# Optimization experiments

Measured on AMD Instinct MI355X. Metric: run time of the kernel, lower is better.

## Reference

```python
import jax, jax.numpy as jnp
import numpy as np

B, S, E, H, D, L, V, O = 64, 512, 512, 8, 64, 4, 50000, 1000
KW, STRIDE = 5, 5
L_OUT = (S - KW) // STRIDE + 1  # 102


def setup_inputs() -> dict:
    key = jax.random.key(0)
    ks = jax.random.split(key, 20)
    sc = 0.02
    inp = {
        'tokens': jax.random.randint(ks[0], (B, S), 0, V, dtype=jnp.int32),
        'emb': jax.random.normal(ks[1], (V + 1, E), jnp.float32) * sc,
        'Wq': jax.random.normal(ks[2], (L, H, E, D), jnp.float32) * sc,
        'bq': jnp.zeros((L, H, D), jnp.float32),
        'Wk': jax.random.normal(ks[3], (L, H, E, D), jnp.float32) * sc,
        'bk': jnp.zeros((L, H, D), jnp.float32),
        'Wv': jax.random.normal(ks[4], (L, H, E, D), jnp.float32) * sc,
        'bv': jnp.zeros((L, H, D), jnp.float32),
        'Wo': jax.random.normal(ks[5], (L, H * D, E), jnp.float32) * sc,
        'bo': jnp.zeros((L, E), jnp.float32),
        'W1': jax.random.normal(ks[6], (L, E, 2 * E), jnp.float32) * sc,
        'b1': jnp.zeros((L, 2 * E), jnp.float32),
        'W2': jax.random.normal(ks[7], (L, 2 * E, E), jnp.float32) * sc,
        'b2': jnp.zeros((L, E), jnp.float32),
        'Wc': jax.random.normal(ks[8], (KW, E, 1), jnp.float32) * sc,
        'bc': jnp.zeros((1,), jnp.float32),
        'Wd': jax.random.normal(ks[9], (L_OUT, O), jnp.float32) * sc,
        'bd': jnp.zeros((O,), jnp.float32),
    }
    return inp


def _l2_normalize(x, eps=1e-12):
    # tf.math.l2_normalize: x / sqrt(max(sum(x^2), eps))
    sq = jnp.sum(x * x, axis=-1, keepdims=True)
    return x * jax.lax.rsqrt(jnp.maximum(sq, eps))


def _forward(tokens, emb, Wq, bq, Wk, bk, Wv, bv, Wo, bo, W1, b1, W2, b2, Wc, bc, Wd, bd):
    mask = jnp.sign(tokens).astype(jnp.float32)[..., None]  # [B,S,1]
    out = emb[tokens] * mask                                 # [B,S,E]
    scale = 1.0 / jnp.sqrt(jnp.float32(E))                   # note: scaled by EMBEDDING_DIM, as in source
    for i in range(L):
        # per-head QKV projections, batched over heads
        q = jnp.einsum('bse,hed->bhsd', out, Wq[i]) + bq[i][None, :, None, :]
        k = jnp.einsum('bse,hed->bhsd', out, Wk[i]) + bk[i][None, :, None, :]
        v = jnp.einsum('bse,hed->bhsd', out, Wv[i]) + bv[i][None, :, None, :]
        scores = jnp.einsum('bhsd,bhtd->bhst', q, k) * scale
        attn = jax.nn.softmax(scores, axis=-1)
        heads = jnp.einsum('bhst,bhtd->bhsd', attn, v)       # [B,H,S,D]
        cat = heads.transpose(0, 2, 1, 3).reshape(B, S, H * D)
        mh = cat @ Wo[i] + bo[i]
        out = _l2_normalize(out + mh)
        ff = jax.nn.relu(out @ W1[i] + b1[i]) @ W2[i] + b2[i]
        out = ff + out
    # Conv1D(1, 5, strides=5) then squeeze channel, Dense over seq-length axis, softmax
    conv = jax.lax.conv_general_dilated(
        out, Wc, window_strides=(STRIDE,), padding='VALID',
        dimension_numbers=('NWC', 'WIO', 'NWC')) + bc          # [B,L_OUT,1]
    pooled = jnp.squeeze(conv, axis=-1)                        # [B,L_OUT]
    logits = pooled @ Wd + bd                                  # [B,O]
    return jax.nn.softmax(logits, axis=-1)


def reference(tokens, emb, Wq, bq, Wk, bk, Wv, bv, Wo, bo, W1, b1, W2, b2, Wc, bc, Wd, bd):
    return _forward(tokens, emb, Wq, bq, Wk, bk, Wv, bv, Wo, bo, W1, b1, W2, b2, Wc, bc, Wd, bd)
```

## Files before the change

kernel.cpp:

```cpp
#include <hip/hip_runtime.h>
#include <cstddef>

constexpr int B_ = 64, S_ = 512, E_ = 512, H_ = 8, D_ = 64, L_ = 4, O_ = 1000;
constexpr int BS_ = B_ * S_;
constexpr int HD_ = H_ * D_;
constexpr int QS_ = 1536;
constexpr int LOUT_ = 102;
constexpr float SCALE_ = 0.04419417382415922f;

typedef __bf16 bf16x8 __attribute__((ext_vector_type(8)));
typedef __bf16 bf16x4 __attribute__((ext_vector_type(4)));
typedef __bf16 bf16x2 __attribute__((ext_vector_type(2)));
typedef float floatx4 __attribute__((ext_vector_type(4)));

__device__ inline void load16_lds(const __bf16* g, __bf16* l) {
  __builtin_amdgcn_global_load_lds(
      (const __attribute__((address_space(1))) void*)g,
      (__attribute__((address_space(3))) void*)l, 16, 0, 0);
}

__global__ __launch_bounds__(256) void transpose_bf16(
    const float* __restrict__ in, __bf16* __restrict__ out,
    int R, int C, int IZ, int OZL, int OZH) {
  __shared__ float t[32][33];
  int z = blockIdx.z;
  const float* inz = in + (size_t)z * IZ;
  __bf16* outz = out + (size_t)(z >> 3) * OZL + (size_t)(z & 7) * OZH;
  int c0 = blockIdx.x * 32, r0 = blockIdx.y * 32;
  int x = threadIdx.x, y = threadIdx.y;
#pragma unroll
  for (int j = 0; j < 32; j += 8) t[y + j][x] = inz[(size_t)(r0 + y + j) * C + c0 + x];
  __syncthreads();
#pragma unroll
  for (int j = 0; j < 32; j += 8)
    outz[(size_t)(c0 + y + j) * R + r0 + x] = (__bf16)t[x][y + j];
}

__global__ __launch_bounds__(256) void bias_concat(
    const float* __restrict__ bq, const float* __restrict__ bk,
    const float* __restrict__ bv, float* __restrict__ qkvb) {
  int idx = blockIdx.x * 256 + threadIdx.x;
  int l = idx / QS_, j = idx % QS_;
  float v;
  if (j < 512) v = bq[l * 512 + j];
  else if (j < 1024) v = bk[l * 512 + j - 512];
  else v = bv[l * 512 + j - 1024];
  qkvb[idx] = v;
}

__global__ __launch_bounds__(256) void embed_kernel(
    const int* __restrict__ tokens, const float* __restrict__ emb,
    float* __restrict__ X, __bf16* __restrict__ Ab) {
  int idx = blockIdx.x * 256 + threadIdx.x;
  int bs = idx >> 7;
  int e = (idx & 127) << 2;
  int tok = tokens[bs];
  float4 v;
  if (tok == 0) v = make_float4(0.f, 0.f, 0.f, 0.f);
  else v = *(const float4*)(emb + (size_t)tok * E_ + e);
  size_t off = (size_t)bs * E_ + e;
  *(float4*)(X + off) = v;
  bf16x4 b;
  b[0] = (__bf16)v.x; b[1] = (__bf16)v.y; b[2] = (__bf16)v.z; b[3] = (__bf16)v.w;
  *(bf16x4*)(Ab + off) = b;
}

template <int RELU, int RES, int OUTF, int OUTB, int SCQ, int KITER>
__global__ __launch_bounds__(256) void gemm_bf16(
    const __bf16* __restrict__ A, const __bf16* __restrict__ Bt,
    const float* __restrict__ bias, const float* __restrict__ Rsd,
    float* __restrict__ Cf, __bf16* __restrict__ Cb, int N, int lda, int Nt) {
  __shared__ __align__(16) __bf16 smem[128 * 136];
  __bf16* As = smem;
  __bf16* Bs = smem + 8192;
  int tid = threadIdx.x;
  int lane = tid & 63, w = tid >> 6;
  int Mt8 = (int)(gridDim.x / Nt) >> 3;
  int xcd = blockIdx.x & 7;
  int j = blockIdx.x >> 3;
  int rr = j % (2 * Nt), chunk = j / (2 * Nt);
  int mt = xcd * Mt8 + chunk * 2 + (rr & 1);
  int nt = rr >> 1;
  int m0 = mt * 128, n0 = nt * 128;
  int q4 = lane >> 4, a_ = lane & 15;
  floatx4 acc[4][4];
#pragma unroll
  for (int i = 0; i < 4; ++i)
#pragma unroll
    for (int jj = 0; jj < 4; ++jj) acc[i][jj] = (floatx4)(0.0f);

  for (int kk = 0; kk < KITER; ++kk) {
    int k0 = kk * 64;
#pragma unroll
    for (int jj = 0; jj < 4; ++jj) {
      int ci = (jj * 4 + w) * 64 + lane;
      int row = ci >> 3, c = ci & 7, q = c ^ (row & 7);
      load16_lds(A + (size_t)(m0 + row) * lda + k0 + q * 8, As + (size_t)(jj * 4 + w) * 512);
    }
#pragma unroll
    for (int jj = 0; jj < 4; ++jj) {
      int ci = (jj * 4 + w) * 64 + lane;
      int row = ci >> 3, c = ci & 7, q = c ^ (row & 7);
      load16_lds(Bt + (size_t)(n0 + row) * (KITER * 64) + k0 + q * 8,
                 Bs + (size_t)(jj * 4 + w) * 512);
    }
    __syncthreads();
#pragma unroll
    for (int ks = 0; ks < 2; ++ks) {
      bf16x8 af[4], bfr[4];
#pragma unroll
      for (int i = 0; i < 4; ++i) {
        int row = (w & 1) * 64 + i * 16 + a_;
        int q = ks * 4 + q4;
        af[i] = *(const bf16x8*)&As[(row * 8 + (q ^ (row & 7))) * 8];
      }
#pragma unroll
      for (int jc = 0; jc < 4; ++jc) {
        int row = (w >> 1) * 64 + jc * 16 + a_;
        int q = ks * 4 + q4;
        bfr[jc] = *(const bf16x8*)&Bs[(row * 8 + (q ^ (row & 7))) * 8];
      }
#pragma unroll
      for (int i = 0; i < 4; ++i)
#pragma unroll
        for (int jc = 0; jc < 4; ++jc)
          acc[i][jc] = __builtin_amdgcn_mfma_f32_16x16x32_bf16(bfr[jc], af[i],
                                                               acc[i][jc], 0, 0, 0);
    }
    __syncthreads();
  }
#pragma unroll
  for (int i = 0; i < 4; ++i) {
    int ml = (w & 1) * 64 + i * 16 + a_;
    int m = m0 + ml;
#pragma unroll
    for (int jc = 0; jc < 4; ++jc) {
      int nl = (w >> 1) * 64 + jc * 16 + q4 * 4;
      int n = n0 + nl;
      float4 bi = *(const float4*)(bias + n);
      floatx4 v = acc[i][jc];
      v[0] += bi.x; v[1] += bi.y; v[2] += bi.z; v[3] += bi.w;
      if (SCQ) { if (n < 512) v *= SCALE_; }
      if (RES) {
        float4 rv = *(const float4*)(Rsd + (size_t)m * N + n);
        v[0] += rv.x; v[1] += rv.y; v[2] += rv.z; v[3] += rv.w;
      }
      if (RELU) {
#pragma unroll
        for (int r = 0; r < 4; ++r) v[r] = fmaxf(v[r], 0.f);
      }
      if (OUTF) {
        float4 o = make_float4(v[0], v[1], v[2], v[3]);
        *(float4*)(Cf + (size_t)m * N + n) = o;
      }
      if (OUTB) {
        bf16x4 ob;
#pragma unroll
        for (int r = 0; r < 4; ++r) ob[r] = (__bf16)v[r];
        *(bf16x4*)&smem[ml * 136 + nl] = ob;
      }
    }
  }
  if (OUTB) {
    __syncthreads();
#pragma unroll
    for (int it = 0; it < 8; ++it) {
      int cid = it * 256 + tid;
      int row = cid >> 4, c8 = cid & 15;
      bf16x8 val = *(const bf16x8*)&smem[row * 136 + c8 * 8];
      *(bf16x8*)(Cb + (size_t)(m0 + row) * N + n0 + c8 * 8) = val;
    }
  }
}

__global__ __launch_bounds__(256, 2) void attn_bf16(__bf16* __restrict__ QKV) {
  __shared__ __align__(16) __bf16 Qs[256 * 64];
  __shared__ __align__(16) __bf16 Ks[64 * 64];
  __shared__ __align__(16) __bf16 Vt[64 * 64];
  __shared__ __align__(16) __bf16 Ps[64 * 64];
  int tid = threadIdx.x, lane = tid & 63, w = tid >> 6;
  int q4 = lane >> 4, a_ = lane & 15;
  int s0 = blockIdx.x * 256, h = blockIdx.y, b = blockIdx.z;
  size_t rowbase = (size_t)b * S_ * QS_ + h * 64;
  __bf16* Qg = QKV + rowbase;
  const __bf16* Kg = QKV + rowbase + 512;
  const __bf16* Vg = QKV + rowbase + 1024;
#pragma unroll
  for (int j = 0; j < 8; ++j) {
    int ci = j * 256 + w * 64 + lane;
    int row = ci >> 3, c = ci & 7, q = c ^ (row & 7);
    load16_lds(Qg + (size_t)(s0 + row) * QS_ + q * 8, Qs + (j * 256 + w * 64) * 8);
  }
  float mrow[4], lrow[4];
  floatx4 accO[4][4];
#pragma unroll
  for (int cc = 0; cc < 4; ++cc) {
    mrow[cc] = -3.0e38f; lrow[cc] = 0.f;
#pragma unroll
    for (int jc = 0; jc < 4; ++jc) accO[cc][jc] = (floatx4)(0.0f);
  }

  for (int t0 = 0; t0 < S_; t0 += 64) {
#pragma unroll
    for (int j = 0; j < 2; ++j) {
      int ci = j * 256 + w * 64 + lane;
      int row = ci >> 3, c = ci & 7, q = c ^ (row & 7);
      load16_lds(Kg + (size_t)(t0 + row) * QS_ + q * 8, Ks + (j * 256 + w * 64) * 8);
    }
    {
      int tp = tid & 31, dg = tid >> 5;
      bf16x8 v0 = *(const bf16x8*)(Vg + (size_t)(t0 + 2 * tp) * QS_ + dg * 8);
      bf16x8 v1 = *(const bf16x8*)(Vg + (size_t)(t0 + 2 * tp + 1) * QS_ + dg * 8);
#pragma unroll
      for (int x = 0; x < 8; ++x) {
        int d = dg * 8 + x;
        bf16x2 p; p[0] = v0[x]; p[1] = v1[x];
        *(bf16x2*)&Vt[(d * 8 + ((tp >> 2) ^ (d & 7))) * 8 + (tp & 3) * 2] = p;
      }
    }
    __syncthreads();
    bf16x8 af[2][4], bv[2][4];
#pragma unroll
    for (int ks = 0; ks < 2; ++ks)
#pragma unroll
      for (int jc = 0; jc < 4; ++jc) {
        int row = jc * 16 + a_, q = ks * 4 + q4;
        af[ks][jc] = *(const bf16x8*)&Ks[(row * 8 + (q ^ (row & 7))) * 8];
        bv[ks][jc] = *(const bf16x8*)&Vt[(row * 8 + (q ^ (row & 7))) * 8];
      }
#pragma unroll
    for (int cc = 0; cc < 4; ++cc) {
      int sbase = (cc * 4 + w) * 16;
      floatx4 sc[4];
#pragma unroll
      for (int jc = 0; jc < 4; ++jc) sc[jc] = (floatx4)(0.0f);
#pragma unroll
      for (int ks = 0; ks < 2; ++ks) {
        int row = sbase + a_, q = ks * 4 + q4;
        bf16x8 bq = *(const bf16x8*)&Qs[(row * 8 + (q ^ (row & 7))) * 8];
#pragma unroll
        for (int jc = 0; jc < 4; ++jc)
          sc[jc] = __builtin_amdgcn_mfma_f32_16x16x32_bf16(af[ks][jc], bq,
                                                           sc[jc], 0, 0, 0);
      }
      float mx = sc[0][0];
#pragma unroll
      for (int jc = 0; jc < 4; ++jc)
#pragma unroll
        for (int r = 0; r < 4; ++r) mx = fmaxf(mx, sc[jc][r]);
      mx = fmaxf(mx, __shfl_xor(mx, 16));
      mx = fmaxf(mx, __shfl_xor(mx, 32));
      float mnew = fmaxf(mrow[cc], mx);
      float alpha = __expf(mrow[cc] - mnew);
      mrow[cc] = mnew;
      float ps = 0.f;
      int prow = w * 16 + a_;
#pragma unroll
      for (int jc = 0; jc < 4; ++jc) {
        bf16x4 pb;
#pragma unroll
        for (int r = 0; r < 4; ++r) {
          float p = __expf(sc[jc][r] - mnew);
          ps += p;
          pb[r] = (__bf16)p;
        }
        int pc = jc * 2 + (q4 >> 1);
        *(bf16x4*)&Ps[(prow * 8 + (pc ^ (prow & 7))) * 8 + (q4 & 1) * 4] = pb;
      }
      ps += __shfl_xor(ps, 16);
      ps += __shfl_xor(ps, 32);
      lrow[cc] = lrow[cc] * alpha + ps;
      float aal[4];
#pragma unroll
      for (int r = 0; r < 4; ++r) aal[r] = __shfl(alpha, q4 * 4 + r);
#pragma unroll
      for (int jc = 0; jc < 4; ++jc) {
        floatx4 t = accO[cc][jc];
#pragma unroll
        for (int r = 0; r < 4; ++r) t[r] *= aal[r];
        accO[cc][jc] = t;
      }
#pragma unroll
      for (int ks = 0; ks < 2; ++ks) {
        int q = ks * 4 + q4;
        bf16x8 ap = *(const bf16x8*)&Ps[(prow * 8 + (q ^ (prow & 7))) * 8];
#pragma unroll
        for (int jc = 0; jc < 4; ++jc)
          accO[cc][jc] = __builtin_amdgcn_mfma_f32_16x16x32_bf16(
              ap, bv[ks][jc], accO[cc][jc], 0, 0, 0);
      }
    }
    __syncthreads();
  }
#pragma unroll
  for (int cc = 0; cc < 4; ++cc) {
    float inv = 1.f / lrow[cc];
    float linv[4];
#pragma unroll
    for (int r = 0; r < 4; ++r) linv[r] = __shfl(inv, q4 * 4 + r);
    int srow = s0 + (cc * 4 + w) * 16 + q4 * 4;
#pragma unroll
    for (int r = 0; r < 4; ++r)
#pragma unroll
      for (int jc = 0; jc < 4; ++jc)
        Qg[(size_t)(srow + r) * QS_ + jc * 16 + a_] =
            (__bf16)(accO[cc][jc][r] * linv[r]);
  }
}

__global__ __launch_bounds__(256) void addnorm_kernel(
    float* __restrict__ X, const __bf16* __restrict__ MH, __bf16* __restrict__ Ab) {
  int row = blockIdx.x * 4 + (threadIdx.x >> 6);
  int ln = threadIdx.x & 63;
  size_t off = (size_t)row * E_ + ln * 8;
  float xv[8];
  *(float4*)&xv[0] = *(const float4*)(X + off);
  *(float4*)&xv[4] = *(const float4*)(X + off + 4);
  bf16x8 mh = *(const bf16x8*)(MH + off);
  float ss = 0.f;
#pragma unroll
  for (int j = 0; j < 8; ++j) {
    xv[j] += (float)mh[j];
    ss += xv[j] * xv[j];
  }
#pragma unroll
  for (int o = 1; o < 64; o <<= 1) ss += __shfl_xor(ss, o);
  float inv = rsqrtf(fmaxf(ss, 1e-12f));
  bf16x8 ob;
#pragma unroll
  for (int j = 0; j < 8; ++j) {
    xv[j] *= inv;
    ob[j] = (__bf16)xv[j];
  }
  *(float4*)(X + off) = *(float4*)&xv[0];
  *(float4*)(X + off + 4) = *(float4*)&xv[4];
  *(bf16x8*)(Ab + off) = ob;
}

__global__ __launch_bounds__(256) void conv_pool_kernel(
    const float* __restrict__ X, const float* __restrict__ Wc,
    const float* __restrict__ bc, float* __restrict__ pooled) {
  int wid = blockIdx.x * 4 + (threadIdx.x >> 6);
  int ln = threadIdx.x & 63;
  int b = wid / LOUT_, l = wid % LOUT_;
  const float* xr = X + (size_t)b * S_ * E_ + (size_t)l * 5 * E_;
  float v = 0.f;
#pragma unroll
  for (int j = 0; j < 10; ++j) {
    int i = (j * 64 + ln) * 4;
    float4 x4 = *(const float4*)(xr + i);
    float4 w4 = *(const float4*)(Wc + i);
    v += x4.x * w4.x + x4.y * w4.y + x4.z * w4.z + x4.w * w4.w;
  }
#pragma unroll
  for (int o = 32; o >= 1; o >>= 1) v += __shfl_down(v, o);
  if (ln == 0) pooled[b * LOUT_ + l] = v + bc[0];
}

__global__ __launch_bounds__(256) void dense_softmax_kernel(
    const float* __restrict__ pooled, const float* __restrict__ Wd,
    const float* __restrict__ bd, float* __restrict__ out) {
  __shared__ float pl[LOUT_];
  __shared__ float red[256];
  __shared__ float lg[O_];
  int b = blockIdx.x, tid = threadIdx.x;
  if (tid < LOUT_) pl[tid] = pooled[b * LOUT_ + tid];
  __syncthreads();
  for (int o = tid; o < O_; o += 256) {
    float acc = bd[o];
#pragma unroll 6
    for (int l = 0; l < LOUT_; ++l) acc += pl[l] * Wd[l * O_ + o];
    lg[o] = acc;
  }
  __syncthreads();
  float mx = -3.0e38f;
  for (int o = tid; o < O_; o += 256) mx = fmaxf(mx, lg[o]);
  red[tid] = mx;
  __syncthreads();
  for (int s2 = 128; s2 > 0; s2 >>= 1) {
    if (tid < s2) red[tid] = fmaxf(red[tid], red[tid + s2]);
    __syncthreads();
  }
  mx = red[0];
  __syncthreads();
  float se = 0.f;
  for (int o = tid; o < O_; o += 256) {
    float e = __expf(lg[o] - mx);
    lg[o] = e;
    se += e;
  }
  red[tid] = se;
  __syncthreads();
  for (int s2 = 128; s2 > 0; s2 >>= 1) {
    if (tid < s2) red[tid] += red[tid + s2];
    __syncthreads();
  }
  float inv = 1.f / red[0];
  for (int o = tid; o < O_; o += 256) out[(size_t)b * O_ + o] = lg[o] * inv;
}

extern "C" void kernel_launch(void* const* d_in, const int* in_sizes, int n_in,
                              void* d_out, int out_size, void* d_ws, size_t ws_size,
                              hipStream_t stream) {
  const int* tokens = (const int*)d_in[0];
  const float* emb = (const float*)d_in[1];
  const float* Wq = (const float*)d_in[2];
  const float* bq = (const float*)d_in[3];
  const float* Wk = (const float*)d_in[4];
  const float* bk = (const float*)d_in[5];
  const float* Wv = (const float*)d_in[6];
  const float* bv = (const float*)d_in[7];
  const float* Wo = (const float*)d_in[8];
  const float* bo = (const float*)d_in[9];
  const float* W1 = (const float*)d_in[10];
  const float* b1 = (const float*)d_in[11];
  const float* W2 = (const float*)d_in[12];
  const float* b2 = (const float*)d_in[13];
  const float* Wc = (const float*)d_in[14];
  const float* bc = (const float*)d_in[15];
  const float* Wd = (const float*)d_in[16];
  const float* bd = (const float*)d_in[17];
  float* out = (float*)d_out;

  char* ws = (char*)d_ws;
  float* X = (float*)ws;
  __bf16* Ab = (__bf16*)(ws + 67108864);
  __bf16* QKVb = (__bf16*)(ws + 100663296);
  __bf16* FF1b = QKVb;
  __bf16* MHb = (__bf16*)(ws + 201326592);
  __bf16* Wt = (__bf16*)(ws + 234881024);
  __bf16* Wt_qkv = Wt;
  __bf16* Wt_o = Wt + 3145728;
  __bf16* Wt_1 = Wt + 4194304;
  __bf16* Wt_2 = Wt + 6291456;
  float* qkvbias = (float*)(ws + 251658240);
  float* pooled = qkvbias + 6144;

  dim3 tb(32, 8);
  transpose_bf16<<<dim3(2, 16, 32), tb, 0, stream>>>(Wq, Wt_qkv + 0,      512, 64, 32768, 786432, 32768);
  transpose_bf16<<<dim3(2, 16, 32), tb, 0, stream>>>(Wk, Wt_qkv + 262144, 512, 64, 32768, 786432, 32768);
  transpose_bf16<<<dim3(2, 16, 32), tb, 0, stream>>>(Wv, Wt_qkv + 524288, 512, 64, 32768, 786432, 32768);
  transpose_bf16<<<dim3(16, 16, 4), tb, 0, stream>>>(Wo, Wt_o, 512, 512, 262144, 0, 262144);
  transpose_bf16<<<dim3(32, 16, 4), tb, 0, stream>>>(W1, Wt_1, 512, 1024, 524288, 0, 524288);
  transpose_bf16<<<dim3(16, 32, 4), tb, 0, stream>>>(W2, Wt_2, 1024, 512, 524288, 0, 524288);
  bias_concat<<<dim3(24), dim3(256), 0, stream>>>(bq, bk, bv, qkvbias);

  embed_kernel<<<dim3(BS_ * E_ / 4 / 256), dim3(256), 0, stream>>>(tokens, emb, X, Ab);

  dim3 blk(256);
  for (int i = 0; i < L_; ++i) {
    gemm_bf16<0, 0, 0, 1, 1, 8><<<dim3(256 * 12), blk, 0, stream>>>(
        Ab, Wt_qkv + (size_t)i * 786432, qkvbias + i * QS_, nullptr, nullptr,
        QKVb, QS_, 512, 12);
    attn_bf16<<<dim3(2, 8, 64), blk, 0, stream>>>(QKVb);
    gemm_bf16<0, 0, 0, 1, 0, 8><<<dim3(256 * 4), blk, 0, stream>>>(
        QKVb, Wt_o + (size_t)i * 262144, bo + i * E_, nullptr, nullptr, MHb,
        512, QS_, 4);
    addnorm_kernel<<<dim3(BS_ / 4), blk, 0, stream>>>(X, MHb, Ab);
    gemm_bf16<1, 0, 0, 1, 0, 8><<<dim3(256 * 8), blk, 0, stream>>>(
        Ab, Wt_1 + (size_t)i * 524288, b1 + (size_t)i * 2 * E_, nullptr, nullptr,
        FF1b, 1024, 512, 8);
    gemm_bf16<0, 1, 1, 1, 0, 16><<<dim3(256 * 4), blk, 0, stream>>>(
        FF1b, Wt_2 + (size_t)i * 524288, b2 + (size_t)i * E_, X, X, Ab,
        512, 1024, 4);
  }
  conv_pool_kernel<<<dim3(BS_ * LOUT_ / S_ / 4), blk, 0, stream>>>(X, Wc, bc, pooled);
  dense_softmax_kernel<<<dim3(B_), blk, 0, stream>>>(pooled, Wd, bd, out);
}
```

Baseline: 1.509 ms.

## Triple-buffer GEMM LDS tiles with async prefetch and K-step of 32

Restructures the bf16 GEMM main loop into a three-stage LDS ring buffer with BK=32 tiles. Loads for tile k+2 are issued via global_load_lds before computing tile k, and explicit vmcnt waits replace the two full syncthreads per iteration. The intent is to overlap global-to-LDS traffic with MFMA work instead of stalling on each load. In exchange there are twice as many K iterations with fewer MFMAs each, and a new XOR swizzle on a 4-chunk row layout.

```diff
diff --git a/kernel.cpp b/kernel.cpp
--- a/kernel.cpp
+++ b/kernel.cpp
@@ -65,14 +65,12 @@
   *(bf16x4*)(Ab + off) = b;
 }
 
-template <int RELU, int RES, int OUTF, int OUTB, int SCQ, int KITER>
+template <int RELU, int RES, int OUTF, int OUTB, int SCQ, int KT>
 __global__ __launch_bounds__(256) void gemm_bf16(
     const __bf16* __restrict__ A, const __bf16* __restrict__ Bt,
     const float* __restrict__ bias, const float* __restrict__ Rsd,
     float* __restrict__ Cf, __bf16* __restrict__ Cb, int N, int lda, int Nt) {
-  __shared__ __align__(16) __bf16 smem[128 * 136];
-  __bf16* As = smem;
-  __bf16* Bs = smem + 8192;
+  __shared__ __align__(16) __bf16 smem[24576];
   int tid = threadIdx.x;
   int lane = tid & 63, w = tid >> 6;
   int Mt8 = (int)(gridDim.x / Nt) >> 3;
@@ -83,51 +81,65 @@
   int nt = rr >> 1;
   int m0 = mt * 128, n0 = nt * 128;
   int q4 = lane >> 4, a_ = lane & 15;
+  const int ldb = KT * 32;
+  int r0s = tid >> 2, q0s = (tid & 3) ^ ((r0s >> 1) & 3);
+  int r1s = 64 + (tid >> 2), q1s = (tid & 3) ^ ((r1s >> 1) & 3);
+  const __bf16* Ag = A + (size_t)m0 * lda;
+  const __bf16* Bg = Bt + (size_t)n0 * ldb;
+
   floatx4 acc[4][4];
 #pragma unroll
   for (int i = 0; i < 4; ++i)
 #pragma unroll
     for (int jj = 0; jj < 4; ++jj) acc[i][jj] = (floatx4)(0.0f);
 
-  for (int kk = 0; kk < KITER; ++kk) {
-    int k0 = kk * 64;
-#pragma unroll
-    for (int jj = 0; jj < 4; ++jj) {
-      int ci = (jj * 4 + w) * 64 + lane;
-      int row = ci >> 3, c = ci & 7, q = c ^ (row & 7);
-      load16_lds(A + (size_t)(m0 + row) * lda + k0 + q * 8, As + (size_t)(jj * 4 + w) * 512);
-    }
-#pragma unroll
-    for (int jj = 0; jj < 4; ++jj) {
-      int ci = (jj * 4 + w) * 64 + lane;
-      int row = ci >> 3, c = ci & 7, q = c ^ (row & 7);
-      load16_lds(Bt + (size_t)(n0 + row) * (KITER * 64) + k0 + q * 8,
-                 Bs + (size_t)(jj * 4 + w) * 512);
-    }
-    __syncthreads();
-#pragma unroll
-    for (int ks = 0; ks < 2; ++ks) {
-      bf16x8 af[4], bfr[4];
-#pragma unroll
-      for (int i = 0; i < 4; ++i) {
-        int row = (w & 1) * 64 + i * 16 + a_;
-        int q = ks * 4 + q4;
-        af[i] = *(const bf16x8*)&As[(row * 8 + (q ^ (row & 7))) * 8];
-      }
-#pragma unroll
-      for (int jc = 0; jc < 4; ++jc) {
-        int row = (w >> 1) * 64 + jc * 16 + a_;
-        int q = ks * 4 + q4;
-        bfr[jc] = *(const bf16x8*)&Bs[(row * 8 + (q ^ (row & 7))) * 8];
-      }
-#pragma unroll
-      for (int i = 0; i < 4; ++i)
-#pragma unroll
-        for (int jc = 0; jc < 4; ++jc)
-          acc[i][jc] = __builtin_amdgcn_mfma_f32_16x16x32_bf16(bfr[jc], af[i],
-                                                               acc[i][jc], 0, 0, 0);
-    }
-    __syncthreads();
+  auto STAGE = [&](int kt, int bs) {
+    __bf16* Ad = smem + bs * 4096;
+    __bf16* Bd = smem + 12288 + bs * 4096;
+    int k0 = kt * 32;
+    load16_lds(Ag + (size_t)r0s * lda + k0 + q0s * 8, Ad + tid * 8);
+    load16_lds(Ag + (size_t)r1s * lda + k0 + q1s * 8, Ad + (256 + tid) * 8);
+    load16_lds(Bg + (size_t)r0s * ldb + k0 + q0s * 8, Bd + tid * 8);
+    load16_lds(Bg + (size_t)r1s * ldb + k0 + q1s * 8, Bd + (256 + tid) * 8);
+  };
+
+  STAGE(0, 0);
+  if (KT > 1) STAGE(1, 1);
+#pragma unroll
+  for (int kt = 0; kt < KT; ++kt) {
+    if (kt + 2 < KT) {
+      STAGE(kt + 2, (kt + 2) % 3);
+      asm volatile("s_waitcnt vmcnt(8)" ::: "memory");
+    } else if (kt + 1 < KT) {
+      asm volatile("s_waitcnt vmcnt(4)" ::: "memory");
+    } else {
+      asm volatile("s_waitcnt vmcnt(0)" ::: "memory");
+    }
+    __builtin_amdgcn_s_barrier();
+    __builtin_amdgcn_sched_barrier(0);
+    const __bf16* As = smem + (kt % 3) * 4096;
+    const __bf16* Bs = smem + 12288 + (kt % 3) * 4096;
+    bf16x8 af[4], bfr[4];
+#pragma unroll
+    for (int i = 0; i < 4; ++i) {
+      int row = (w & 1) * 64 + i * 16 + a_;
+      int pc = q4 ^ ((row >> 1) & 3);
+      af[i] = *(const bf16x8*)&As[(row * 4 + pc) * 8];
+    }
+#pragma unroll
+    for (int jc = 0; jc < 4; ++jc) {
+      int row = (w >> 1) * 64 + jc * 16 + a_;
+      int pc = q4 ^ ((row >> 1) & 3);
+      bfr[jc] = *(const bf16x8*)&Bs[(row * 4 + pc) * 8];
+    }
+#pragma unroll
+    for (int i = 0; i < 4; ++i)
+#pragma unroll
+      for (int jc = 0; jc < 4; ++jc)
+        acc[i][jc] = __builtin_amdgcn_mfma_f32_16x16x32_bf16(bfr[jc], af[i],
+                                                             acc[i][jc], 0, 0, 0);
+    asm volatile("" ::: "memory");
+    __builtin_amdgcn_s_barrier();
   }
 #pragma unroll
   for (int i = 0; i < 4; ++i) {
@@ -449,18 +461,18 @@
 
   dim3 blk(256);
   for (int i = 0; i < L_; ++i) {
-    gemm_bf16<0, 0, 0, 1, 1, 8><<<dim3(256 * 12), blk, 0, stream>>>(
+    gemm_bf16<0, 0, 0, 1, 1, 16><<<dim3(256 * 12), blk, 0, stream>>>(
         Ab, Wt_qkv + (size_t)i * 786432, qkvbias + i * QS_, nullptr, nullptr,
         QKVb, QS_, 512, 12);
     attn_bf16<<<dim3(2, 8, 64), blk, 0, stream>>>(QKVb);
-    gemm_bf16<0, 0, 0, 1, 0, 8><<<dim3(256 * 4), blk, 0, stream>>>(
+    gemm_bf16<0, 0, 0, 1, 0, 16><<<dim3(256 * 4), blk, 0, stream>>>(
         QKVb, Wt_o + (size_t)i * 262144, bo + i * E_, nullptr, nullptr, MHb,
         512, QS_, 4);
     addnorm_kernel<<<dim3(BS_ / 4), blk, 0, stream>>>(X, MHb, Ab);
-    gemm_bf16<1, 0, 0, 1, 0, 8><<<dim3(256 * 8), blk, 0, stream>>>(
+    gemm_bf16<1, 0, 0, 1, 0, 16><<<dim3(256 * 8), blk, 0, stream>>>(
         Ab, Wt_1 + (size_t)i * 524288, b1 + (size_t)i * 2 * E_, nullptr, nullptr,
         FF1b, 1024, 512, 8);
-    gemm_bf16<0, 1, 1, 1, 0, 16><<<dim3(256 * 4), blk, 0, stream>>>(
+    gemm_bf16<0, 1, 1, 1, 0, 32><<<dim3(256 * 4), blk, 0, stream>>>(
         FF1b, Wt_2 + (size_t)i * 524288, b2 + (size_t)i * E_, X, X, Ab,
         512, 1024, 4);
   }
```

Result: faster. 1.392 ms (-7.8%).
